# Performance work log

Measured on AMD Instinct MI355X. Metric: run time of the kernel, lower is better.

The kernel has to match this reference:

```python
import jax, jax.numpy as jnp
import numpy as np
import math

B, C, L, D = 64, 21, 8192, 512
KG, KP = 25, 15  # gaussian decomp kernel, phase-corrector kernel (both odd)
PI = math.pi


def _reflect_pad(x, k):
    # x: [B, C, T]; torch 'same' reflect padding: left = k//2, right = k-1-k//2
    pl = k // 2
    return jnp.pad(x, ((0, 0), (0, 0), (pl, k - 1 - pl)), mode='reflect')


def _depthwise_conv1d(x, w):
    # x: [B, C, T_pad], w: [C, 1, k]  (cross-correlation, groups=C, VALID)
    return jax.lax.conv_general_dilated(
        x, w, window_strides=(1,), padding='VALID',
        dimension_numbers=('NCH', 'OIH', 'NCH'),
        feature_group_count=x.shape[1])


def _phase_unwrap(phase):
    # phase: [B, L, C]; unwrap along time axis=1 (matches torch implementation)
    d = jnp.diff(phase, axis=1)
    d_mod = jnp.mod(d + PI, 2.0 * PI) - PI
    d_mod = jnp.where((d_mod == -PI) & (d > 0), PI, d_mod)
    correction = jnp.cumsum(d_mod - d, axis=1)
    return jnp.concatenate([phase[:, :1, :], phase[:, 1:, :] + correction], axis=1)


def _analytic_signal(x):
    # scipy.signal.hilbert along axis=1; x: [B, L, C], L even
    n = x.shape[1]
    h = np.zeros(n, dtype=np.float32)
    h[0] = 1.0
    h[n // 2] = 1.0
    h[1:n // 2] = 2.0
    Xf = jnp.fft.fft(x, axis=1)
    return jnp.fft.ifft(Xf * jnp.asarray(h)[None, :, None], axis=1)


def setup_inputs() -> dict:
    key = jax.random.key(0)
    ks = jax.random.split(key, 4)
    return {
        'x_input': jax.random.normal(ks[0], (B, C, L), jnp.float32),
        'x_w': jax.random.normal(ks[1], (L, D), jnp.float32) / np.sqrt(L).astype(np.float32),
        'x_b': jnp.zeros((D,), jnp.float32),
        'i_w': jax.random.normal(ks[2], (L, D), jnp.float32) / np.sqrt(L).astype(np.float32),
        'i_b': jnp.zeros((D,), jnp.float32),
        'log_sigma': jnp.full((C,), math.log(3.0), jnp.float32),
        'pc_weight': jax.random.normal(ks[3], (C, 1, KP), jnp.float32) * 0.01,
        'pc_strength': jnp.asarray(0.2, jnp.float32),
        'alpha_log': jnp.zeros((C,), jnp.float32),
        'phi0': jnp.zeros((C,), jnp.float32),
        'beta1_log': jnp.asarray(0.0, jnp.float32),
        'beta2_log': jnp.asarray(0.0, jnp.float32),
    }


def reference(x_input, x_w, x_b, i_w, i_b, log_sigma, pc_weight, pc_strength,
              alpha_log, phi0, beta1_log, beta2_log):
    # x_input: [B, C, L]
    x_out = jax.nn.gelu(x_input @ x_w + x_b, approximate=False)  # [B, C, D]

    # --- decomp_Gaussian (depthwise gaussian low-pass) ---
    half = KG // 2
    idx = jnp.arange(-half, half + 1, dtype=x_input.dtype)
    sigma = jnp.exp(log_sigma)[:, None, None] + 1e-6            # [C,1,1]
    g = jnp.exp(-(idx[None, None, :] ** 2) / (2.0 * sigma * sigma))
    g = g / (g.sum(axis=-1, keepdims=True) + 1e-12)             # [C,1,KG]
    trend_ch = _depthwise_conv1d(_reflect_pad(x_input, KG), g)  # [B,C,L]
    seasonal = (x_input - trend_ch).transpose(0, 2, 1)          # [B,L,C]
    trend = trend_ch.transpose(0, 2, 1)                         # [B,L,C]

    # --- TSCoupler ---
    # hilbert_transform uses .detach() in the original -> stop_gradient
    z = _analytic_signal(jax.lax.stop_gradient(seasonal))
    phase = jnp.arctan2(z.imag, z.real)                         # [B,L,C]
    phase_u = _phase_unwrap(phase)

    # ZeroMeanPhaseCorrector
    w = pc_weight - pc_weight.mean(axis=-1, keepdims=True)
    delta = _depthwise_conv1d(_reflect_pad(phase_u.transpose(0, 2, 1), KP), w)
    phi_corr = phase_u + jnp.tanh(pc_strength) * delta.transpose(0, 2, 1)
    phi_corr = phi_corr + phi0[None, None, :]

    T_clamped = jnp.clip(trend, -10.0, 10.0)
    beta1 = jax.nn.softplus(beta1_log) + 1e-6
    beta2 = jax.nn.softplus(beta2_log) + 1e-6
    A_raw = beta1 * jnp.log1p(jnp.exp(beta2 * T_clamped))       # [B,L,C]
    alpha = jax.nn.softplus(alpha_log)[None, None, :] + 1e-6    # [1,1,C]
    A_t = alpha * A_raw[0]                                      # [1,L,C]  (batch-0 indexing, as in source)
    I = (A_t * jnp.cos(phi_corr)).transpose(0, 2, 1)            # [B,C,L]

    I_coupled = jax.nn.gelu(I @ i_w + i_b, approximate=False)   # [B,C,D]
    return (x_out, I_coupled)
```

## Files before the change

kernel.cpp:

```cpp
#include <hip/hip_runtime.h>
#include <hip/hip_bf16.h>
#include <math.h>

#define LMAX 8192
#define KGAUSS 25

#define PI_F 3.14159265358979323846f
#define TWO_PI_F 6.28318530717958647692f

typedef __hip_bfloat16 bf16;
typedef unsigned short u16;
typedef short bf16x8 __attribute__((ext_vector_type(8)));
typedef float f32x4 __attribute__((ext_vector_type(4)));

__device__ __forceinline__ float b2f(bf16 v) { return __bfloat162float(v); }
__device__ __forceinline__ bf16 f2b(float v) { return __float2bfloat16(v); }
__device__ __forceinline__ float rdv(const void* p, long i, int isb) {
  return isb ? b2f(((const bf16*)p)[i]) : ((const float*)p)[i];
}

__device__ __forceinline__ void async16(const void* g, void* l) {
#if __has_builtin(__builtin_amdgcn_global_load_lds)
  __builtin_amdgcn_global_load_lds((const __attribute__((address_space(1))) void*)g,
                                   (__attribute__((address_space(3))) void*)l, 16, 0, 0);
#else
  *(uint4*)l = *(const uint4*)g;
#endif
}

__device__ __forceinline__ float2 f2add(float2 a, float2 b) {
  return make_float2(a.x + b.x, a.y + b.y);
}
__device__ __forceinline__ float2 f2sub(float2 a, float2 b) {
  return make_float2(a.x - b.x, a.y - b.y);
}
__device__ __forceinline__ float2 cmulc(float2 x, float2 w) {
  return make_float2(x.x * w.x + x.y * w.y, x.y * w.x - x.x * w.y);
}
__device__ __forceinline__ float2 cmul(float2 x, float2 w) {
  return make_float2(x.x * w.x - x.y * w.y, x.x * w.y + x.y * w.x);
}
#define ZI(i) ((i) ^ (((i) >> 4) & 15))
#define XS(i) ((i) ^ (((i) >> 5) & 31))

__global__ void k_params(const void* xb, const void* ib, const void* ls, const void* pw,
                         const void* al, const void* ph, const void* ps, const void* b1,
                         const void* b2, float* pf, int* flag, float2* tw,
                         int D, int C, int KP, int L) {
  unsigned wls = ((const unsigned*)ls)[0];
  int isb = ((wls >> 16) == (wls & 0xffffu)) ? 1 : 0;
  int blk = blockIdx.x, t = threadIdx.x;
  if (blk < 64) {
    int i = blk * 256 + t;
    if (i == 0) flag[0] = isb;
    float v = 0.0f;
    if (i < D)                              v = rdv(xb, i, isb);
    else if (i >= 2048 && i < 2048 + D)     v = rdv(ib, i - 2048, isb);
    else if (i >= 4096 && i < 4096 + C)     v = rdv(ls, i - 4096, isb);
    else if (i >= 4352 && i < 4352 + C*KP)  v = rdv(pw, i - 4352, isb);
    else if (i >= 8448 && i < 8448 + C)     v = rdv(al, i - 8448, isb);
    else if (i >= 8704 && i < 8704 + C)     v = rdv(ph, i - 8704, isb);
    else if (i == 8960)                     v = rdv(ps, 0, isb);
    else if (i == 8961)                     v = rdv(b1, 0, isb);
    else if (i == 8962)                     v = rdv(b2, 0, isb);
    pf[i] = v;
  } else {
    int j = (blk - 64) * 256 + t;
    if (j < L / 2) {
      double a = 6.283185307179586476925286766559 * (double)j / (double)L;
      tw[j] = make_float2((float)cos(a), (float)sin(a));
    }
  }
}

__global__ __launch_bounds__(256) void k_transpose(const void* __restrict__ in,
    bf16* __restrict__ out, const int* __restrict__ flag, int K, int N) {
  __shared__ u16 tile[64][65];
  int isb = *flag;
  int r0 = blockIdx.x * 64, c0 = blockIdx.y * 64;
  int t = threadIdx.x;
#pragma unroll
  for (int i = 0; i < 16; ++i) {
    int idx = t + i * 256;
    int r = idx >> 6, cc = idx & 63;
    int gr = r0 + r; gr = gr < K ? gr : K - 1;
    int gc = c0 + cc; gc = gc < N ? gc : N - 1;
    size_t gi = (size_t)gr * N + gc;
    u16 v;
    if (isb) v = ((const u16*)in)[gi];
    else { bf16 h = f2b(((const float*)in)[gi]); v = *(u16*)&h; }
    tile[r][cc] = v;
  }
  __syncthreads();
#pragma unroll
  for (int i = 0; i < 16; ++i) {
    int idx = t + i * 256;
    int a = idx >> 6, bb = idx & 63;
    if (c0 + a < N && r0 + bb < K)
      ((u16*)out)[(size_t)(c0 + a) * K + (r0 + bb)] = tile[bb][a];
  }
}

__global__ __launch_bounds__(256, 4) void k_decomp32(const void* __restrict__ x,
    const int* __restrict__ flag, const float* __restrict__ pf,
    float* __restrict__ seasonal, float* __restrict__ trend0,
    bf16* __restrict__ Xb, int C, int L) {
  __shared__ float xs[LMAX + LMAX / 32];
  int bc = blockIdx.x, c = bc % C, b = bc / C;
  int t = threadIdx.x;
  int isb = *flag;
  for (int i = t; i < L; i += 256) {
    float xv = rdv(x, (size_t)bc * L + i, isb);
    xs[i + (i >> 5)] = xv;
    Xb[(size_t)bc * L + i] = f2b(xv);
  }
  float sigma = expf(pf[4096 + c]) + 1e-6f;
  float inv2s2 = 1.0f / (2.0f * sigma * sigma);
  float g[KGAUSS];
  float gs = 0.0f;
#pragma unroll
  for (int j = 0; j < KGAUSS; ++j) {
    float d = (float)(j - 12);
    float vv = expf(-(d * d) * inv2s2);
    g[j] = vv; gs += vv;
  }
  float ginv = 1.0f / (gs + 1e-12f);
#pragma unroll
  for (int j = 0; j < KGAUSS; ++j) g[j] *= ginv;
  __syncthreads();
  const int base = 32 * t;
  float v[56];
#pragma unroll
  for (int m = 0; m < 56; ++m) {
    int idx = base + m - 12;
    idx = idx < 0 ? -idx : (idx >= L ? 2 * L - 2 - idx : idx);
    v[m] = xs[idx + (idx >> 5)];
  }
  __syncthreads();
  const int sb = 33 * t;
  float aA = 0.0f, ab1 = 0.0f, ab2 = 0.0f;
  if (b == 0) {
    aA  = log1pf(expf(pf[8448 + c])) + 1e-6f;
    ab1 = log1pf(expf(pf[8961])) + 1e-6f;
    ab2 = log1pf(expf(pf[8962])) + 1e-6f;
  }
  float* trow = trend0 + (size_t)c * L;
#pragma unroll
  for (int ii = 0; ii < 32; ++ii) {
    float acc = 0.0f;
#pragma unroll
    for (int j = 0; j < KGAUSS; ++j) acc = fmaf(g[j], v[ii + j], acc);
    xs[sb + ii] = v[ii + 12] - acc;
    if (b == 0) {
      float T = fminf(10.0f, fmaxf(-10.0f, acc));
      trow[base + ii] = aA * (ab1 * log1pf(expf(ab2 * T)));
    }
  }
  __syncthreads();
  for (int i = t; i < L; i += 256)
    seasonal[(size_t)bc * L + i] = xs[i + (i >> 5)];
}

__global__ __launch_bounds__(256) void k_decomp(const void* __restrict__ x,
    const int* __restrict__ flag, const float* __restrict__ pf,
    float* __restrict__ seasonal, float* __restrict__ trend0,
    bf16* __restrict__ Xb, int C, int L) {
  __shared__ float xs[LMAX];
  int bc = blockIdx.x;
  int c = bc % C, b = bc / C;
  int t = threadIdx.x;
  int isb = *flag;
  for (int i = t; i < L; i += 256) {
    float xv = rdv(x, (size_t)bc * L + i, isb);
    xs[i] = xv;
    Xb[(size_t)bc * L + i] = f2b(xv);
  }
  float sigma = expf(pf[4096 + c]) + 1e-6f;
  float inv2s2 = 1.0f / (2.0f * sigma * sigma);
  float g[KGAUSS];
  float gs = 0.0f;
  for (int j = 0; j < KGAUSS; ++j) {
    float d = (float)(j - 12);
    float v = expf(-(d * d) * inv2s2);
    g[j] = v; gs += v;
  }
  float ginv = 1.0f / (gs + 1e-12f);
  for (int j = 0; j < KGAUSS; ++j) g[j] *= ginv;
  float aA  = log1pf(expf(pf[8448 + c])) + 1e-6f;
  float ab1 = log1pf(expf(pf[8961])) + 1e-6f;
  float ab2 = log1pf(expf(pf[8962])) + 1e-6f;
  __syncthreads();
  for (int i = t; i < L; i += 256) {
    float acc = 0.0f;
#pragma unroll
    for (int j = 0; j < KGAUSS; ++j) {
      int idx = i + j - 12;
      idx = idx < 0 ? -idx : (idx >= L ? 2 * L - 2 - idx : idx);
      acc += g[j] * xs[idx];
    }
    seasonal[(size_t)bc * L + i] = xs[i] - acc;
    if (b == 0) {
      float T = fminf(10.0f, fmaxf(-10.0f, acc));
      trend0[(size_t)c * L + i] = aA * (ab1 * log1pf(expf(ab2 * T)));
    }
  }
}

__global__ __launch_bounds__(512, 4) void k_hilbert_unwrap(
    const float* __restrict__ sp, const float2* __restrict__ tw,
    const float* __restrict__ amp, const float* __restrict__ pf,
    bf16* __restrict__ I, int C, int L, int lg, long M) {
  __shared__ float2 z[LMAX];
  float* P = (float*)z;
  long r0 = 2L * blockIdx.x;
  int has1 = (r0 + 1 < M) ? 1 : 0;
  const float* row0 = sp + (size_t)r0 * L;
  const float* row1 = row0 + (has1 ? (size_t)L : 0);
  const int t = threadIdx.x;
  const int T = 512;
  const int nq = L >> 3;

  for (int s = lg; s >= 4; s -= 3) {
    const int h4 = 1 << (s - 3);
    for (int q = t; q < nq; q += T) {
      int pos = q & (h4 - 1);
      int base = ((q >> (s - 3)) << s) + pos;
      float2 E0, E1, E2, E3, E4, E5, E6, E7;
      if (s == lg) {
        int i;
        i = base;          E0 = make_float2(row0[i], has1 ? row1[i] : 0.0f);
        i = base + h4;     E1 = make_float2(row0[i], has1 ? row1[i] : 0.0f);
        i = base + 2*h4;   E2 = make_float2(row0[i], has1 ? row1[i] : 0.0f);
        i = base + 3*h4;   E3 = make_float2(row0[i], has1 ? row1[i] : 0.0f);
        i = base + 4*h4;   E4 = make_float2(row0[i], has1 ? row1[i] : 0.0f);
        i = base + 5*h4;   E5 = make_float2(row0[i], has1 ? row1[i] : 0.0f);
        i = base + 6*h4;   E6 = make_float2(row0[i], has1 ? row1[i] : 0.0f);
        i = base + 7*h4;   E7 = make_float2(row0[i], has1 ? row1[i] : 0.0f);
      } else {
        E0 = z[ZI(base)];          E1 = z[ZI(base + h4)];
        E2 = z[ZI(base + 2*h4)];   E3 = z[ZI(base + 3*h4)];
        E4 = z[ZI(base + 4*h4)];   E5 = z[ZI(base + 5*h4)];
        E6 = z[ZI(base + 6*h4)];   E7 = z[ZI(base + 7*h4)];
      }
      float2 wa0 = tw[pos << (lg - s)];
      float2 wa1 = tw[(pos + h4) << (lg - s)];
      float2 wa2 = tw[(pos + 2*h4) << (lg - s)];
      float2 wa3 = tw[(pos + 3*h4) << (lg - s)];
      float2 wb0 = tw[pos << (lg - s + 1)];
      float2 wb1 = tw[(pos + h4) << (lg - s + 1)];
      float2 wc0 = tw[pos << (lg - s + 2)];
      float2 A0 = f2add(E0, E4), B0 = cmulc(f2sub(E0, E4), wa0);
      float2 A1 = f2add(E1, E5), B1 = cmulc(f2sub(E1, E5), wa1);
      float2 A2 = f2add(E2, E6), B2 = cmulc(f2sub(E2, E6), wa2);
      float2 A3 = f2add(E3, E7), B3 = cmulc(f2sub(E3, E7), wa3);
      float2 C0 = f2add(A0, A2), C2 = cmulc(f2sub(A0, A2), wb0);
      float2 C1 = f2add(A1, A3), C3 = cmulc(f2sub(A1, A3), wb1);
      float2 D0 = f2add(B0, B2), D2 = cmulc(f2sub(B0, B2), wb0);
      float2 D1 = f2add(B1, B3), D3 = cmulc(f2sub(B1, B3), wb1);
      z[ZI(base)]          = f2add(C0, C1);
      z[ZI(base + h4)]     = cmulc(f2sub(C0, C1), wc0);
      z[ZI(base + 2*h4)]   = f2add(C2, C3);
      z[ZI(base + 3*h4)]   = cmulc(f2sub(C2, C3), wc0);
      z[ZI(base + 4*h4)]   = f2add(D0, D1);
      z[ZI(base + 5*h4)]   = cmulc(f2sub(D0, D1), wc0);
      z[ZI(base + 6*h4)]   = f2add(D2, D3);
      z[ZI(base + 7*h4)]   = cmulc(f2sub(D2, D3), wc0);
    }
    __syncthreads();
  }
  {
    const float s1 = 1.0f / (float)L, s2 = 2.0f / (float)L;
    const int h = L >> 1;
    for (int q = t; q < (L >> 1); q += T) {
      int i0 = 2 * q, i1 = i0 + 1;
      float2 a = z[ZI(i0)], b = z[ZI(i1)];
      float2 u0 = f2add(a, b), u1 = f2sub(a, b);
      int k0 = (int)(__brev((unsigned)i0) >> (32 - lg));
      int k1 = (int)(__brev((unsigned)i1) >> (32 - lg));
      float sc0 = (k0 == 0 || k0 == h) ? s1 : (k0 < h ? s2 : 0.0f);
      float sc1 = (k1 == 0 || k1 == h) ? s1 : (k1 < h ? s2 : 0.0f);
      u0.x *= sc0; u0.y *= sc0; u1.x *= sc1; u1.y *= sc1;
      z[ZI(i0)] = f2add(u0, u1);
      z[ZI(i1)] = f2sub(u0, u1);
    }
  }
  __syncthreads();
  for (int s = 2; s + 2 <= lg - 3; s += 3) {
    const int h = 1 << (s - 1);
    for (int q = t; q < nq; q += T) {
      int pos = q & (h - 1);
      int base = ((q >> (s - 1)) << (s + 2)) + pos;
      float2 E0 = z[ZI(base)],         E1 = z[ZI(base + h)];
      float2 E2 = z[ZI(base + 2*h)],   E3 = z[ZI(base + 3*h)];
      float2 E4 = z[ZI(base + 4*h)],   E5 = z[ZI(base + 5*h)];
      float2 E6 = z[ZI(base + 6*h)],   E7 = z[ZI(base + 7*h)];
      float2 w0  = tw[pos << (lg - s)];
      float2 w10 = tw[pos << (lg - s - 1)];
      float2 w11 = tw[(pos + h) << (lg - s - 1)];
      float2 w20 = tw[pos << (lg - s - 2)];
      float2 w21 = tw[(pos + h) << (lg - s - 2)];
      float2 w22 = tw[(pos + 2*h) << (lg - s - 2)];
      float2 w23 = tw[(pos + 3*h) << (lg - s - 2)];
      float2 c;
      c = cmul(E1, w0); float2 A0 = f2add(E0, c), A1 = f2sub(E0, c);
      c = cmul(E3, w0); float2 A2 = f2add(E2, c), A3 = f2sub(E2, c);
      c = cmul(E5, w0); float2 A4 = f2add(E4, c), A5 = f2sub(E4, c);
      c = cmul(E7, w0); float2 A6 = f2add(E6, c), A7 = f2sub(E6, c);
      c = cmul(A2, w10); float2 B0 = f2add(A0, c), B2 = f2sub(A0, c);
      c = cmul(A3, w11); float2 B1 = f2add(A1, c), B3 = f2sub(A1, c);
      c = cmul(A6, w10); float2 B4 = f2add(A4, c), B6 = f2sub(A4, c);
      c = cmul(A7, w11); float2 B5 = f2add(A5, c), B7 = f2sub(A5, c);
      float2 F0, F1, F2, F3, F4, F5, F6, F7;
      c = cmul(B4, w20); F0 = f2add(B0, c); F4 = f2sub(B0, c);
      c = cmul(B5, w21); F1 = f2add(B1, c); F5 = f2sub(B1, c);
      c = cmul(B6, w22); F2 = f2add(B2, c); F6 = f2sub(B2, c);
      c = cmul(B7, w23); F3 = f2add(B3, c); F7 = f2sub(B3, c);
      z[ZI(base)]        = F0; z[ZI(base + h)]    = F1;
      z[ZI(base + 2*h)]  = F2; z[ZI(base + 3*h)]  = F3;
      z[ZI(base + 4*h)]  = F4; z[ZI(base + 5*h)]  = F5;
      z[ZI(base + 6*h)]  = F6; z[ZI(base + 7*h)]  = F7;
    }
    __syncthreads();
  }
  {
    const int s = lg - 2;
    const int h = 1 << (s - 1);
    float2 Ea[2][8];
    int bs[2];
#pragma unroll
    for (int it = 0; it < 2; ++it) {
      int q = t + it * T;
      int pos = q & (h - 1);
      int base = ((q >> (s - 1)) << (s + 2)) + pos;
      bs[it] = base;
      Ea[it][0] = z[ZI(base)];         Ea[it][1] = z[ZI(base + h)];
      Ea[it][2] = z[ZI(base + 2*h)];   Ea[it][3] = z[ZI(base + 3*h)];
      Ea[it][4] = z[ZI(base + 4*h)];   Ea[it][5] = z[ZI(base + 5*h)];
      Ea[it][6] = z[ZI(base + 6*h)];   Ea[it][7] = z[ZI(base + 7*h)];
    }
    __syncthreads();
#pragma unroll
    for (int it = 0; it < 2; ++it) {
      int q = t + it * T;
      int pos = q & (h - 1);
      int base = bs[it];
      float2 w0  = tw[pos << (lg - s)];
      float2 w10 = tw[pos << (lg - s - 1)];
      float2 w11 = tw[(pos + h) << (lg - s - 1)];
      float2 w20 = tw[pos << (lg - s - 2)];
      float2 w21 = tw[(pos + h) << (lg - s - 2)];
      float2 w22 = tw[(pos + 2*h) << (lg - s - 2)];
      float2 w23 = tw[(pos + 3*h) << (lg - s - 2)];
      float2 c;
      c = cmul(Ea[it][1], w0); float2 A0 = f2add(Ea[it][0], c), A1 = f2sub(Ea[it][0], c);
      c = cmul(Ea[it][3], w0); float2 A2 = f2add(Ea[it][2], c), A3 = f2sub(Ea[it][2], c);
      c = cmul(Ea[it][5], w0); float2 A4 = f2add(Ea[it][4], c), A5 = f2sub(Ea[it][4], c);
      c = cmul(Ea[it][7], w0); float2 A6 = f2add(Ea[it][6], c), A7 = f2sub(Ea[it][6], c);
      c = cmul(A2, w10); float2 B0 = f2add(A0, c), B2 = f2sub(A0, c);
      c = cmul(A3, w11); float2 B1 = f2add(A1, c), B3 = f2sub(A1, c);
      c = cmul(A6, w10); float2 B4 = f2add(A4, c), B6 = f2sub(A4, c);
      c = cmul(A7, w11); float2 B5 = f2add(A5, c), B7 = f2sub(A5, c);
      float2 F[8];
      c = cmul(B4, w20); F[0] = f2add(B0, c); F[4] = f2sub(B0, c);
      c = cmul(B5, w21); F[1] = f2add(B1, c); F[5] = f2sub(B1, c);
      c = cmul(B6, w22); F[2] = f2add(B2, c); F[6] = f2sub(B2, c);
      c = cmul(B7, w23); F[3] = f2add(B3, c); F[7] = f2sub(B3, c);
#pragma unroll
      for (int j = 0; j < 8; ++j) {
        int i = base + j * h;
        float xa = row0[i];
        float xb = has1 ? row1[i] : 0.0f;
        float ha = F[j].y - xb;
        float hb = xa - F[j].x;
        P[XS(i)] = atan2f(ha, xa);
        P[L + XS(i)] = has1 ? atan2f(hb, xb) : 0.0f;
      }
    }
  }
  __syncthreads();
  {
    int tr = t & 255, row = t >> 8;
    int rowoff = row ? L : 0;
    int c = (int)((r0 + row) % C);
    int sb32 = 32 * tr;
    float v[32];
#pragma unroll
    for (int ii = 0; ii < 32; ++ii) v[ii] = P[rowoff + XS(sb32 + ii)];
    float prev0 = (tr > 0) ? P[rowoff + XS(sb32 - 1)] : 0.0f;
    __syncthreads();
    int run = 0;
    {
      float prev = prev0;
#pragma unroll
      for (int ii = 0; ii < 32; ++ii) {
        float cur = v[ii];
        if (ii > 0 || tr > 0) {
          float d = cur - prev;
          int k = (int)floorf((d + PI_F) * (1.0f / TWO_PI_F));
          float m = d - TWO_PI_F * (float)k;
          if (m == -PI_F && d > 0.0f) k -= 1;
          run -= k;
        }
        prev = cur;
        v[ii] = cur + TWO_PI_F * (float)run;
      }
    }
    int lane = t & 63, w = t >> 6;
    int inc = run;
#pragma unroll
    for (int off2 = 1; off2 < 64; off2 <<= 1) {
      int n = __shfl_up(inc, off2);
      if (lane >= off2) inc += n;
    }
    int* iP = (int*)P;
    if (lane == 63) iP[w] = inc;
    __syncthreads();
    int base = inc - run;
    int rowbase = row * 4;
    for (int ww = rowbase; ww < w; ++ww) base += iP[ww];
    __syncthreads();
    float fb = TWO_PI_F * (float)base;
#pragma unroll
    for (int ii = 0; ii < 32; ++ii) v[ii] += fb;
#pragma unroll
    for (int ii = 0; ii < 32; ++ii) P[rowoff + XS(sb32 + ii)] = v[ii];
    __syncthreads();
    float hl[7], hr[7];
#pragma unroll
    for (int m = 0; m < 7; ++m)
      hl[m] = (tr == 0) ? v[7 - m] : P[rowoff + XS(sb32 - 7 + m)];
#pragma unroll
    for (int m = 0; m < 7; ++m)
      hr[m] = (tr == 255) ? v[30 - m] : P[rowoff + XS(sb32 + 32 + m)];
    __syncthreads();
    float wz[15];
    float mean = 0.0f;
#pragma unroll
    for (int j = 0; j < 15; ++j) { wz[j] = pf[4352 + c * 15 + j]; mean += wz[j]; }
    mean *= (1.0f / 15.0f);
#pragma unroll
    for (int j = 0; j < 15; ++j) wz[j] -= mean;
    float tanh_s = tanhf(pf[8960]);
    float phi0c = pf[8704 + c];
#pragma unroll
    for (int ii = 0; ii < 32; ++ii) {
      float delta = 0.0f;
#pragma unroll
      for (int j = 0; j < 15; ++j) {
        int idx = ii + j - 7;
        float u = (idx < 0) ? hl[idx + 7] : (idx >= 32 ? hr[idx - 32] : v[idx]);
        delta = fmaf(wz[j], u, delta);
      }
      float phi = v[ii] + tanh_s * delta + phi0c;
      P[rowoff + XS(sb32 + ii)] = cosf(phi);
    }
    __syncthreads();
    const float* ar0 = amp + (size_t)(r0 % C) * L;
    const float* ar1 = amp + (size_t)((r0 + 1) % C) * L;
    bf16* I0 = I + (size_t)r0 * L;
    bf16* I1 = I0 + L;
    for (int i = t; i < L; i += 512) {
      I0[i] = f2b(ar0[i] * P[XS(i)]);
      if (has1) I1[i] = f2b(ar1[i] * P[L + XS(i)]);
    }
  }
}

__global__ __launch_bounds__(512, 4) void k_hilbert8(float* __restrict__ sp,
    const float2* __restrict__ tw, int L, int lg, long M) {
  __shared__ float2 z[LMAX];
  long r0 = 2L * blockIdx.x;
  int has1 = (r0 + 1 < M) ? 1 : 0;
  float* row0 = sp + (size_t)r0 * L;
  float* row1 = row0 + (has1 ? (size_t)L : 0);
  const int t = threadIdx.x;
  const int T = 512;
  const int nq = L >> 3;

  for (int s = lg; s >= 4; s -= 3) {
    const int h4 = 1 << (s - 3);
    for (int q = t; q < nq; q += T) {
      int pos = q & (h4 - 1);
      int base = ((q >> (s - 3)) << s) + pos;
      float2 E0, E1, E2, E3, E4, E5, E6, E7;
      if (s == lg) {
        int i;
        i = base;          E0 = make_float2(row0[i], has1 ? row1[i] : 0.0f);
        i = base + h4;     E1 = make_float2(row0[i], has1 ? row1[i] : 0.0f);
        i = base + 2*h4;   E2 = make_float2(row0[i], has1 ? row1[i] : 0.0f);
        i = base + 3*h4;   E3 = make_float2(row0[i], has1 ? row1[i] : 0.0f);
        i = base + 4*h4;   E4 = make_float2(row0[i], has1 ? row1[i] : 0.0f);
        i = base + 5*h4;   E5 = make_float2(row0[i], has1 ? row1[i] : 0.0f);
        i = base + 6*h4;   E6 = make_float2(row0[i], has1 ? row1[i] : 0.0f);
        i = base + 7*h4;   E7 = make_float2(row0[i], has1 ? row1[i] : 0.0f);
      } else {
        E0 = z[ZI(base)];          E1 = z[ZI(base + h4)];
        E2 = z[ZI(base + 2*h4)];   E3 = z[ZI(base + 3*h4)];
        E4 = z[ZI(base + 4*h4)];   E5 = z[ZI(base + 5*h4)];
        E6 = z[ZI(base + 6*h4)];   E7 = z[ZI(base + 7*h4)];
      }
      float2 wa0 = tw[pos << (lg - s)];
      float2 wa1 = tw[(pos + h4) << (lg - s)];
      float2 wa2 = tw[(pos + 2*h4) << (lg - s)];
      float2 wa3 = tw[(pos + 3*h4) << (lg - s)];
      float2 wb0 = tw[pos << (lg - s + 1)];
      float2 wb1 = tw[(pos + h4) << (lg - s + 1)];
      float2 wc0 = tw[pos << (lg - s + 2)];
      float2 A0 = f2add(E0, E4), B0 = cmulc(f2sub(E0, E4), wa0);
      float2 A1 = f2add(E1, E5), B1 = cmulc(f2sub(E1, E5), wa1);
      float2 A2 = f2add(E2, E6), B2 = cmulc(f2sub(E2, E6), wa2);
      float2 A3 = f2add(E3, E7), B3 = cmulc(f2sub(E3, E7), wa3);
      float2 C0 = f2add(A0, A2), C2 = cmulc(f2sub(A0, A2), wb0);
      float2 C1 = f2add(A1, A3), C3 = cmulc(f2sub(A1, A3), wb1);
      float2 D0 = f2add(B0, B2), D2 = cmulc(f2sub(B0, B2), wb0);
      float2 D1 = f2add(B1, B3), D3 = cmulc(f2sub(B1, B3), wb1);
      z[ZI(base)]          = f2add(C0, C1);
      z[ZI(base + h4)]     = cmulc(f2sub(C0, C1), wc0);
      z[ZI(base + 2*h4)]   = f2add(C2, C3);
      z[ZI(base + 3*h4)]   = cmulc(f2sub(C2, C3), wc0);
      z[ZI(base + 4*h4)]   = f2add(D0, D1);
      z[ZI(base + 5*h4)]   = cmulc(f2sub(D0, D1), wc0);
      z[ZI(base + 6*h4)]   = f2add(D2, D3);
      z[ZI(base + 7*h4)]   = cmulc(f2sub(D2, D3), wc0);
    }
    __syncthreads();
  }
  {
    const float s1 = 1.0f / (float)L, s2 = 2.0f / (float)L;
    const int h = L >> 1;
    for (int q = t; q < (L >> 1); q += T) {
      int i0 = 2 * q, i1 = i0 + 1;
      float2 a = z[ZI(i0)], b = z[ZI(i1)];
      float2 u0 = f2add(a, b), u1 = f2sub(a, b);
      int k0 = (int)(__brev((unsigned)i0) >> (32 - lg));
      int k1 = (int)(__brev((unsigned)i1) >> (32 - lg));
      float sc0 = (k0 == 0 || k0 == h) ? s1 : (k0 < h ? s2 : 0.0f);
      float sc1 = (k1 == 0 || k1 == h) ? s1 : (k1 < h ? s2 : 0.0f);
      u0.x *= sc0; u0.y *= sc0; u1.x *= sc1; u1.y *= sc1;
      z[ZI(i0)] = f2add(u0, u1);
      z[ZI(i1)] = f2sub(u0, u1);
    }
  }
  __syncthreads();
  for (int s = 2; s + 2 <= lg; s += 3) {
    const int h = 1 << (s - 1);
    const int last = (s + 2 == lg) ? 1 : 0;
    for (int q = t; q < nq; q += T) {
      int pos = q & (h - 1);
      int base = ((q >> (s - 1)) << (s + 2)) + pos;
      float2 E0 = z[ZI(base)],         E1 = z[ZI(base + h)];
      float2 E2 = z[ZI(base + 2*h)],   E3 = z[ZI(base + 3*h)];
      float2 E4 = z[ZI(base + 4*h)],   E5 = z[ZI(base + 5*h)];
      float2 E6 = z[ZI(base + 6*h)],   E7 = z[ZI(base + 7*h)];
      float2 w0  = tw[pos << (lg - s)];
      float2 w10 = tw[pos << (lg - s - 1)];
      float2 w11 = tw[(pos + h) << (lg - s - 1)];
      float2 w20 = tw[pos << (lg - s - 2)];
      float2 w21 = tw[(pos + h) << (lg - s - 2)];
      float2 w22 = tw[(pos + 2*h) << (lg - s - 2)];
      float2 w23 = tw[(pos + 3*h) << (lg - s - 2)];
      float2 c;
      c = cmul(E1, w0); float2 A0 = f2add(E0, c), A1 = f2sub(E0, c);
      c = cmul(E3, w0); float2 A2 = f2add(E2, c), A3 = f2sub(E2, c);
      c = cmul(E5, w0); float2 A4 = f2add(E4, c), A5 = f2sub(E4, c);
      c = cmul(E7, w0); float2 A6 = f2add(E6, c), A7 = f2sub(E6, c);
      c = cmul(A2, w10); float2 B0 = f2add(A0, c), B2 = f2sub(A0, c);
      c = cmul(A3, w11); float2 B1 = f2add(A1, c), B3 = f2sub(A1, c);
      c = cmul(A6, w10); float2 B4 = f2add(A4, c), B6 = f2sub(A4, c);
      c = cmul(A7, w11); float2 B5 = f2add(A5, c), B7 = f2sub(A5, c);
      float2 F0, F1, F2, F3, F4, F5, F6, F7;
      c = cmul(B4, w20); F0 = f2add(B0, c); F4 = f2sub(B0, c);
      c = cmul(B5, w21); F1 = f2add(B1, c); F5 = f2sub(B1, c);
      c = cmul(B6, w22); F2 = f2add(B2, c); F6 = f2sub(B2, c);
      c = cmul(B7, w23); F3 = f2add(B3, c); F7 = f2sub(B3, c);
      if (last) {
        float2 ov[8] = {F0, F1, F2, F3, F4, F5, F6, F7};
#pragma unroll
        for (int j = 0; j < 8; ++j) {
          int i = base + j * h;
          float xa = row0[i];
          float xb = has1 ? row1[i] : 0.0f;
          float ha = ov[j].y - xb;
          float hb = xa - ov[j].x;
          row0[i] = atan2f(ha, xa);
          if (has1) row1[i] = atan2f(hb, xb);
        }
      } else {
        z[ZI(base)]        = F0; z[ZI(base + h)]    = F1;
        z[ZI(base + 2*h)]  = F2; z[ZI(base + 3*h)]  = F3;
        z[ZI(base + 4*h)]  = F4; z[ZI(base + 5*h)]  = F5;
        z[ZI(base + 6*h)]  = F6; z[ZI(base + 7*h)]  = F7;
      }
    }
    if (!last) __syncthreads();
  }
}

__global__ __launch_bounds__(512, 4) void k_hilbert4(float* __restrict__ sp,
    const float2* __restrict__ tw, int L, int lg, long M) {
  __shared__ float2 z[LMAX];
  long r0 = 2L * blockIdx.x;
  int has1 = (r0 + 1 < M) ? 1 : 0;
  float* row0 = sp + (size_t)r0 * L;
  float* row1 = row0 + (has1 ? (size_t)L : 0);
  const int t = threadIdx.x;
  const int T = 512;
  const int nq = L >> 2;

  {
    const int s = lg;
    const int h = 1 << (s - 1), h2 = h >> 1;
    for (int q = t; q < nq; q += T) {
      int pos = q & (h2 - 1);
      int base = ((q >> (s - 2)) << s) + pos;
      int i0 = base, i1 = base + h2, i2 = base + h, i3 = base + h + h2;
      float2 e0 = make_float2(row0[i0], has1 ? row1[i0] : 0.0f);
      float2 e1 = make_float2(row0[i1], has1 ? row1[i1] : 0.0f);
      float2 e2 = make_float2(row0[i2], has1 ? row1[i2] : 0.0f);
      float2 e3 = make_float2(row0[i3], has1 ? row1[i3] : 0.0f);
      float2 wa = tw[pos << (lg - s)];
      float2 wb = tw[(pos + h2) << (lg - s)];
      float2 wc = tw[pos << (lg - s + 1)];
      float2 t0 = f2add(e0, e2), t2 = cmulc(f2sub(e0, e2), wa);
      float2 t1 = f2add(e1, e3), t3 = cmulc(f2sub(e1, e3), wb);
      z[ZI(i0)] = f2add(t0, t1);
      z[ZI(i1)] = cmulc(f2sub(t0, t1), wc);
      z[ZI(i2)] = f2add(t2, t3);
      z[ZI(i3)] = cmulc(f2sub(t2, t3), wc);
    }
  }
  __syncthreads();
  for (int s = lg - 2; s >= 2; s -= 2) {
    const int h = 1 << (s - 1), h2 = h >> 1;
    for (int q = t; q < nq; q += T) {
      int pos = q & (h2 - 1);
      int base = ((q >> (s - 2)) << s) + pos;
      int i0 = base, i1 = base + h2, i2 = base + h, i3 = base + h + h2;
      float2 e0 = z[ZI(i0)], e1 = z[ZI(i1)], e2 = z[ZI(i2)], e3 = z[ZI(i3)];
      float2 wa = tw[pos << (lg - s)];
      float2 wb = tw[(pos + h2) << (lg - s)];
      float2 wc = tw[pos << (lg - s + 1)];
      float2 t0 = f2add(e0, e2), t2 = cmulc(f2sub(e0, e2), wa);
      float2 t1 = f2add(e1, e3), t3 = cmulc(f2sub(e1, e3), wb);
      z[ZI(i0)] = f2add(t0, t1);
      z[ZI(i1)] = cmulc(f2sub(t0, t1), wc);
      z[ZI(i2)] = f2add(t2, t3);
      z[ZI(i3)] = cmulc(f2sub(t2, t3), wc);
    }
    __syncthreads();
  }
  {
    const float s1 = 1.0f / (float)L, s2 = 2.0f / (float)L;
    const int h = L >> 1;
    if (lg & 1) {
      for (int q = t; q < (L >> 1); q += T) {
        int i0 = 2 * q, i1 = i0 + 1;
        float2 a = z[ZI(i0)], b = z[ZI(i1)];
        float2 u0 = f2add(a, b), u1 = f2sub(a, b);
        int k0 = (int)(__brev((unsigned)i0) >> (32 - lg));
        int k1 = (int)(__brev((unsigned)i1) >> (32 - lg));
        float sc0 = (k0 == 0 || k0 == h) ? s1 : (k0 < h ? s2 : 0.0f);
        float sc1 = (k1 == 0 || k1 == h) ? s1 : (k1 < h ? s2 : 0.0f);
        u0.x *= sc0; u0.y *= sc0; u1.x *= sc1; u1.y *= sc1;
        z[ZI(i0)] = f2add(u0, u1);
        z[ZI(i1)] = f2sub(u0, u1);
      }
    } else {
      for (int p = t; p < L; p += T) {
        int k = (int)(__brev((unsigned)p) >> (32 - lg));
        float sc = (k == 0 || k == h) ? s1 : (k < h ? s2 : 0.0f);
        float2 v = z[ZI(p)];
        v.x *= sc; v.y *= sc;
        z[ZI(p)] = v;
      }
    }
  }
  __syncthreads();
  const int s0 = (lg & 1) ? 2 : 1;
  for (int s = s0; s + 1 <= lg - 2; s += 2) {
    const int hs = 1 << (s - 1);
    for (int q = t; q < nq; q += T) {
      int pos = q & (hs - 1);
      int base = ((q >> (s - 1)) << (s + 1)) + pos;
      int i0 = base, i1 = base + hs, i2 = base + 2 * hs, i3 = base + 3 * hs;
      float2 e0 = z[ZI(i0)], e1 = z[ZI(i1)], e2 = z[ZI(i2)], e3 = z[ZI(i3)];
      float2 wa = tw[pos << (lg - s)];
      float2 wb = tw[pos << (lg - s - 1)];
      float2 wcc = tw[(pos + hs) << (lg - s - 1)];
      float2 c1 = cmul(e1, wa);
      float2 t0 = f2add(e0, c1), t1 = f2sub(e0, c1);
      float2 d1 = cmul(e3, wa);
      float2 t2 = f2add(e2, d1), t3 = f2sub(e2, d1);
      c1 = cmul(t2, wb);
      float2 o0 = f2add(t0, c1), o2 = f2sub(t0, c1);
      d1 = cmul(t3, wcc);
      float2 o1 = f2add(t1, d1), o3 = f2sub(t1, d1);
      z[ZI(i0)] = o0; z[ZI(i1)] = o1; z[ZI(i2)] = o2; z[ZI(i3)] = o3;
    }
    __syncthreads();
  }
  {
    const int s = lg - 1;
    const int hs = 1 << (s - 1);
    for (int q = t; q < nq; q += T) {
      int pos = q & (hs - 1);
      int base = ((q >> (s - 1)) << (s + 1)) + pos;
      int i0 = base, i1 = base + hs, i2 = base + 2 * hs, i3 = base + 3 * hs;
      float2 e0 = z[ZI(i0)], e1 = z[ZI(i1)], e2 = z[ZI(i2)], e3 = z[ZI(i3)];
      float2 wa = tw[pos << (lg - s)];
      float2 wb = tw[pos << (lg - s - 1)];
      float2 wcc = tw[(pos + hs) << (lg - s - 1)];
      float2 c1 = cmul(e1, wa);
      float2 t0 = f2add(e0, c1), t1 = f2sub(e0, c1);
      float2 d1 = cmul(e3, wa);
      float2 t2 = f2add(e2, d1), t3 = f2sub(e2, d1);
      c1 = cmul(t2, wb);
      float2 o0 = f2add(t0, c1), o2 = f2sub(t0, c1);
      d1 = cmul(t3, wcc);
      float2 o1 = f2add(t1, d1), o3 = f2sub(t1, d1);
      int idx[4] = {i0, i1, i2, i3};
      float2 ov[4] = {o0, o1, o2, o3};
#pragma unroll
      for (int j = 0; j < 4; ++j) {
        int i = idx[j];
        float xa = row0[i];
        float xb = has1 ? row1[i] : 0.0f;
        float2 w = ov[j];
        float ha = w.y - xb;
        float hb = xa - w.x;
        row0[i] = atan2f(ha, xa);
        if (has1) row1[i] = atan2f(hb, xb);
      }
    }
  }
}

__global__ __launch_bounds__(256, 4) void k_unwrap_I32(
    const float* __restrict__ phase_all, const float* __restrict__ amp,
    const float* __restrict__ pf, bf16* __restrict__ I, int C, int L) {
  __shared__ float p[LMAX + LMAX / 32];
  __shared__ int wsum[8];
  int bc = blockIdx.x, c = bc % C;
  int t = threadIdx.x;
  const float* prow = phase_all + (size_t)bc * L;
  for (int i = t; i < L; i += 256) p[i + (i >> 5)] = prow[i];
  __syncthreads();
  const int sbase = 33 * t;
  float v[32];
#pragma unroll
  for (int ii = 0; ii < 32; ++ii) v[ii] = p[sbase + ii];
  float prev = (t > 0) ? p[sbase - 2] : 0.0f;
  int run = 0;
#pragma unroll
  for (int ii = 0; ii < 32; ++ii) {
    float cur = v[ii];
    if (ii > 0 || t > 0) {
      float d = cur - prev;
      int k = (int)floorf((d + PI_F) * (1.0f / TWO_PI_F));
      float m = d - TWO_PI_F * (float)k;
      if (m == -PI_F && d > 0.0f) k -= 1;
      run -= k;
    }
    prev = cur;
    v[ii] = cur + TWO_PI_F * (float)run;
  }
  int lane = t & 63, w = t >> 6;
  int inc = run;
#pragma unroll
  for (int off = 1; off < 64; off <<= 1) {
    int n = __shfl_up(inc, off);
    if (lane >= off) inc += n;
  }
  if (lane == 63) wsum[w] = inc;
  __syncthreads();
  int base = inc - run;
  for (int ww = 0; ww < w; ++ww) base += wsum[ww];
  float fb = TWO_PI_F * (float)base;
#pragma unroll
  for (int ii = 0; ii < 32; ++ii) v[ii] += fb;
#pragma unroll
  for (int ii = 0; ii < 32; ++ii) p[sbase + ii] = v[ii];
  __syncthreads();
  float hl[7], hr[7];
#pragma unroll
  for (int m = 0; m < 7; ++m)
    hl[m] = (t == 0) ? v[7 - m] : p[sbase - 8 + m];
#pragma unroll
  for (int m = 0; m < 7; ++m)
    hr[m] = (t == 255) ? v[30 - m] : p[sbase + 33 + m];
  __syncthreads();
  float wz[15];
  float mean = 0.0f;
#pragma unroll
  for (int j = 0; j < 15; ++j) { wz[j] = pf[4352 + c * 15 + j]; mean += wz[j]; }
  mean /= 15.0f;
#pragma unroll
  for (int j = 0; j < 15; ++j) wz[j] -= mean;
  float tanh_s = tanhf(pf[8960]);
  float phi0c = pf[8704 + c];
#pragma unroll
  for (int ii = 0; ii < 32; ++ii) {
    float delta = 0.0f;
#pragma unroll
    for (int j = 0; j < 15; ++j) {
      int idx = ii + j - 7;
      float u = (idx < 0) ? hl[idx + 7] : (idx >= 32 ? hr[idx - 32] : v[idx]);
      delta = fmaf(wz[j], u, delta);
    }
    float phi = v[ii] + tanh_s * delta + phi0c;
    p[sbase + ii] = cosf(phi);
  }
  __syncthreads();
  const float* arow = amp + (size_t)c * L;
  bf16* Irow = I + (size_t)bc * L;
  for (int i = t; i < L; i += 256)
    Irow[i] = f2b(arow[i] * p[i + (i >> 5)]);
}

__global__ __launch_bounds__(256) void k_unwrap_I(const float* __restrict__ phase_all,
    const float* __restrict__ amp, const float* __restrict__ pf,
    bf16* __restrict__ I, int C, int L, int KP) {
  __shared__ float p[LMAX];
  __shared__ int ksum[256];
  int bc = blockIdx.x;
  int c = bc % C;
  int t = threadIdx.x;
  int chunk = L >> 8;
  const float* prow = phase_all + (size_t)bc * L;
  for (int i = t; i < L; i += 256) p[i] = prow[i];
  __syncthreads();
  int start = t * chunk;
  float prev0 = (t > 0) ? p[start - 1] : 0.0f;
  int kacc = 0;
  {
    float prev = prev0;
    for (int ii = 0; ii < chunk; ++ii) {
      int i = start + ii;
      float cur = p[i];
      if (i > 0) {
        float d = cur - prev;
        int k = (int)floorf((d + PI_F) * (1.0f / TWO_PI_F));
        float m = d - TWO_PI_F * (float)k;
        if (m == -PI_F && d > 0.0f) k -= 1;
        kacc -= k;
      }
      prev = cur;
    }
  }
  ksum[t] = kacc;
  __syncthreads();
  if (t == 0) {
    int run = 0;
    for (int i = 0; i < 256; ++i) { int v = ksum[i]; ksum[i] = run; run += v; }
  }
  __syncthreads();
  {
    int run = ksum[t];
    float prev = prev0;
    for (int ii = 0; ii < chunk; ++ii) {
      int i = start + ii;
      float cur = p[i];
      if (i > 0) {
        float d = cur - prev;
        int k = (int)floorf((d + PI_F) * (1.0f / TWO_PI_F));
        float m = d - TWO_PI_F * (float)k;
        if (m == -PI_F && d > 0.0f) k -= 1;
        run -= k;
      }
      prev = cur;
      p[i] = cur + TWO_PI_F * (float)run;
    }
  }
  __syncthreads();
  float wz[32];
  float mean = 0.0f;
  for (int j = 0; j < KP; ++j) { wz[j] = pf[4352 + c * KP + j]; mean += wz[j]; }
  mean /= (float)KP;
  for (int j = 0; j < KP; ++j) wz[j] -= mean;
  int hk = KP / 2;
  float tanh_s = tanhf(pf[8960]);
  float phi0c = pf[8704 + c];
  const float* arow = amp + (size_t)c * L;
  bf16* Irow = I + (size_t)bc * L;
  for (int i = t; i < L; i += 256) {
    float delta = 0.0f;
    for (int j = 0; j < KP; ++j) {
      int idx = i + j - hk;
      idx = idx < 0 ? -idx : (idx >= L ? 2 * L - 2 - idx : idx);
      delta = fmaf(wz[j], p[idx], delta);
    }
    float phi = p[i] + tanh_s * delta + phi0c;
    Irow[i] = f2b(arow[i] * cosf(phi));
  }
}

__global__ __launch_bounds__(256) void k_gemm_sk(const bf16* __restrict__ A0,
    const bf16* __restrict__ A1, const bf16* __restrict__ B0,
    const bf16* __restrict__ B1, float* __restrict__ part,
    int M, int L, int D, int KS, int KC) {
  __shared__ __align__(16) u16 As[128 * 32];
  __shared__ __align__(16) u16 Bs[128 * 32];
  int zz = blockIdx.z;
  int g = zz / KS, ks = zz - g * KS;
  const u16* Ag = (const u16*)(g ? A1 : A0);
  const u16* Bg = (const u16*)(g ? B1 : B0);
  int m0 = blockIdx.x * 128, n0 = blockIdx.y * 128;
  int t = threadIdx.x;
  int l = t & 63, w = t >> 6;
  int wm = (w >> 1) * 64, wn = (w & 1) * 64;
  int lr = l & 15, lq = l >> 4;
  f32x4 acc[4][4];
  f32x4 z4 = 0.0f;
  for (int i = 0; i < 4; ++i)
    for (int j = 0; j < 4; ++j) acc[i][j] = z4;

  int kbeg = ks * KC, kend = kbeg + KC;
  for (int k0 = kbeg; k0 < kend; k0 += 32) {
#pragma unroll
    for (int q = 0; q < 2; ++q) {
      int chunk = q * 256 + t;
      int row = chunk >> 2, kc = chunk & 3;
      int ar = m0 + row; ar = ar < M ? ar : M - 1;
      int br = n0 + row; br = br < D ? br : D - 1;
      async16(Ag + (size_t)ar * L + (k0 + kc * 8), As + chunk * 8);
      async16(Bg + (size_t)br * L + (k0 + kc * 8), Bs + chunk * 8);
    }
    __syncthreads();
    bf16x8 af[4], bfr[4];
#pragma unroll
    for (int i = 0; i < 4; ++i) {
      af[i]  = *(const bf16x8*)(As + (wm + i * 16 + lr) * 32 + lq * 8);
      bfr[i] = *(const bf16x8*)(Bs + (wn + i * 16 + lr) * 32 + lq * 8);
    }
#pragma unroll
    for (int i = 0; i < 4; ++i)
#pragma unroll
      for (int j = 0; j < 4; ++j)
        acc[i][j] = __builtin_amdgcn_mfma_f32_16x16x32_bf16(af[i], bfr[j], acc[i][j], 0, 0, 0);
    __syncthreads();
  }
  float* pbase = part + (size_t)zz * M * D;
#pragma unroll
  for (int i = 0; i < 4; ++i) {
    int rowb = m0 + wm + i * 16 + lq * 4;
#pragma unroll
    for (int j = 0; j < 4; ++j) {
      int gcol = n0 + wn + j * 16 + lr;
      if (gcol < D) {
#pragma unroll
        for (int r = 0; r < 4; ++r) {
          int grow = rowb + r;
          if (grow < M)
            pbase[(size_t)grow * D + gcol] = acc[i][j][r];
        }
      }
    }
  }
}

__global__ __launch_bounds__(256) void k_reduce(const float* __restrict__ part,
    const float* __restrict__ pf, float* __restrict__ out, long MD, int D, int KS) {
  long idx = (long)blockIdx.x * 256 + threadIdx.x;
  if (idx >= 2 * MD) return;
  int g = (int)(idx / MD);
  long r = idx - (long)g * MD;
  const float* p = part + (size_t)g * KS * MD + r;
  float s = 0.0f;
  for (int ks = 0; ks < KS; ++ks) s += p[(size_t)ks * MD];
  int d = (int)(r % (long)D);
  float v = s + pf[g * 2048 + d];
  out[idx] = 0.5f * v * (1.0f + erff(v * 0.70710678118654752f));
}

static inline int cdiv_i(long a, long b) { return (int)((a + b - 1) / b); }

extern "C" void kernel_launch(void* const* d_in, const int* in_sizes, int n_in,
                              void* d_out, int out_size, void* d_ws, size_t ws_size,
                              hipStream_t stream) {
  long B = 64, C = 21, L = 8192, D = 512, KP = 15;
  if (n_in == 12) {
    long Sx = in_sizes[0], Sw = in_sizes[1], Sb = in_sizes[2];
    long Sls = in_sizes[5], Spw = in_sizes[6];
    if (Sb > 0 && Sw % Sb == 0 && Sls > 0 && Spw % Sls == 0) {
      long Lc = Sw / Sb, KPc = Spw / Sls;
      if (Lc >= 256 && Lc <= LMAX && !(Lc & (Lc - 1)) && (KPc & 1) && KPc <= 31 &&
          Sx % (Sls * Lc) == 0) {
        L = Lc; D = Sb; C = Sls; KP = KPc; B = Sx / (Sls * Lc);
      }
    }
  }
  long M = B * C;
  int lg = 0; while ((1L << lg) < L) ++lg;

  const void* x_input = d_in[0];
  const void* x_w     = d_in[1];
  const void* x_b     = d_in[2];
  const void* i_w     = d_in[3];
  const void* i_b     = d_in[4];
  const void* lsg     = d_in[5];
  const void* pw      = d_in[6];
  const void* ps      = d_in[7];
  const void* al      = d_in[8];
  const void* ph      = d_in[9];
  const void* b1      = d_in[10];
  const void* b2      = d_in[11];

  char* ws = (char*)d_ws;
  size_t off = 0;
  auto take = [&](size_t bytes) { size_t o = off; off = (off + bytes + 255) & ~(size_t)255; return o; };
  float*  seasonal = (float*)(ws + take((size_t)M * L * 4));
  float*  trend0   = (float*)(ws + take((size_t)C * L * 4));
  bf16*   Ibuf     = (bf16*)(ws + take((size_t)M * L * 2));
  float2* tw       = (float2*)(ws + take((size_t)(L / 2) * 8));
  float*  pf       = (float*)(ws + take(65536));
  int*    flag     = (int*)(ws + take(256));
  bf16*   Xb       = (bf16*)(ws + take((size_t)M * L * 2));
  bf16*   Btx      = (bf16*)(ws + take((size_t)D * L * 2));
  bf16*   Bti      = (bf16*)(ws + take((size_t)D * L * 2));
  if (ws_size < off) return;

  int KS = 8;
  while (KS > 1 && ((L % ((long)KS * 32)) != 0 || 2L * KS * D > L)) KS >>= 1;
  float* out0 = (float*)d_out;
  float* part = (2L * KS * D <= L) ? seasonal : out0;
  int KC = (int)(L / KS);

  k_params<<<64 + cdiv_i(L / 2, 256), 256, 0, stream>>>(
      x_b, i_b, lsg, pw, al, ph, ps, b1, b2, pf, flag, tw,
      (int)D, (int)C, (int)KP, (int)L);

  k_transpose<<<dim3(cdiv_i(L, 64), cdiv_i(D, 64)), 256, 0, stream>>>(x_w, Btx, flag,
                                                                      (int)L, (int)D);
  k_transpose<<<dim3(cdiv_i(L, 64), cdiv_i(D, 64)), 256, 0, stream>>>(i_w, Bti, flag,
                                                                      (int)L, (int)D);

  if (L == 8192)
    k_decomp32<<<(int)M, 256, 0, stream>>>(x_input, flag, pf, seasonal, trend0, Xb,
                                           (int)C, (int)L);
  else
    k_decomp<<<(int)M, 256, 0, stream>>>(x_input, flag, pf, seasonal, trend0, Xb,
                                         (int)C, (int)L);

  bool fused = (L == 8192 && KP == 15 && ((lg - 1) % 3 == 0));
  if (fused) {
    k_hilbert_unwrap<<<cdiv_i(M, 2), 512, 0, stream>>>(
        seasonal, tw, trend0, pf, Ibuf, (int)C, (int)L, lg, M);
  } else {
    if ((lg - 1) % 3 == 0)
      k_hilbert8<<<cdiv_i(M, 2), 512, 0, stream>>>(seasonal, tw, (int)L, lg, M);
    else
      k_hilbert4<<<cdiv_i(M, 2), 512, 0, stream>>>(seasonal, tw, (int)L, lg, M);
    if (L == 8192 && KP == 15)
      k_unwrap_I32<<<(int)M, 256, 0, stream>>>(seasonal, trend0, pf, Ibuf, (int)C, (int)L);
    else
      k_unwrap_I<<<(int)M, 256, 0, stream>>>(seasonal, trend0, pf, Ibuf, (int)C, (int)L,
                                             (int)KP);
  }

  k_gemm_sk<<<dim3(cdiv_i(M, 128), cdiv_i(D, 128), 2 * KS), 256, 0, stream>>>(
      Xb, Ibuf, Btx, Bti, part, (int)M, (int)L, (int)D, KS, KC);
  k_reduce<<<cdiv_i(2 * M * D, 256), 256, 0, stream>>>(part, pf, out0, M * D, (int)D, KS);
}
```

Baseline: 374.2 us.

## Double-buffer GEMM LDS tiles, merge weight transposes, vectorize split-K reduce

The split-K GEMM now double-buffers its A/B LDS tiles. The next k-slice's async global-to-LDS loads are issued before computing on the current buffer, and one barrier per iteration is removed. The two weight transpose launches are merged into one launch using blockIdx.z, and the split-K reduction with GELU is vectorized to float4 loads and stores. These target memory latency in the GEMM, launch overhead, and reduce bandwidth efficiency, at the cost of doubled LDS usage per block.

```diff
diff --git a/kernel.cpp b/kernel.cpp
--- a/kernel.cpp
+++ b/kernel.cpp
@@ -73,10 +73,13 @@
   }
 }
 
-__global__ __launch_bounds__(256) void k_transpose(const void* __restrict__ in,
-    bf16* __restrict__ out, const int* __restrict__ flag, int K, int N) {
+__global__ __launch_bounds__(256) void k_transpose2(const void* __restrict__ in0,
+    const void* __restrict__ in1, bf16* __restrict__ out0, bf16* __restrict__ out1,
+    const int* __restrict__ flag, int K, int N) {
   __shared__ u16 tile[64][65];
   int isb = *flag;
+  const void* in = blockIdx.z ? in1 : in0;
+  bf16* out = blockIdx.z ? out1 : out0;
   int r0 = blockIdx.x * 64, c0 = blockIdx.y * 64;
   int t = threadIdx.x;
 #pragma unroll
@@ -898,8 +901,8 @@
     const bf16* __restrict__ A1, const bf16* __restrict__ B0,
     const bf16* __restrict__ B1, float* __restrict__ part,
     int M, int L, int D, int KS, int KC) {
-  __shared__ __align__(16) u16 As[128 * 32];
-  __shared__ __align__(16) u16 Bs[128 * 32];
+  __shared__ __align__(16) u16 As[2][128 * 32];
+  __shared__ __align__(16) u16 Bs[2][128 * 32];
   int zz = blockIdx.z;
   int g = zz / KS, ks = zz - g * KS;
   const u16* Ag = (const u16*)(g ? A1 : A0);
@@ -914,30 +917,37 @@
   for (int i = 0; i < 4; ++i)
     for (int j = 0; j < 4; ++j) acc[i][j] = z4;
 
+  int row = t >> 2, kc = t & 3;
+  int ar = m0 + row; ar = ar < M ? ar : M - 1;
+  int br = n0 + row; br = br < D ? br : D - 1;
+  int row2 = (256 + t) >> 2, kc2 = t & 3;
+  int ar2 = m0 + row2; ar2 = ar2 < M ? ar2 : M - 1;
+  int br2 = n0 + row2; br2 = br2 < D ? br2 : D - 1;
+
   int kbeg = ks * KC, kend = kbeg + KC;
+  auto STAGE = [&](int buf, int k0) {
+    async16(Ag + (size_t)ar * L + (k0 + kc * 8), &As[buf][t * 8]);
+    async16(Bg + (size_t)br * L + (k0 + kc * 8), &Bs[buf][t * 8]);
+    async16(Ag + (size_t)ar2 * L + (k0 + kc2 * 8), &As[buf][(256 + t) * 8]);
+    async16(Bg + (size_t)br2 * L + (k0 + kc2 * 8), &Bs[buf][(256 + t) * 8]);
+  };
+  STAGE(0, kbeg);
+  int cur = 0;
   for (int k0 = kbeg; k0 < kend; k0 += 32) {
-#pragma unroll
-    for (int q = 0; q < 2; ++q) {
-      int chunk = q * 256 + t;
-      int row = chunk >> 2, kc = chunk & 3;
-      int ar = m0 + row; ar = ar < M ? ar : M - 1;
-      int br = n0 + row; br = br < D ? br : D - 1;
-      async16(Ag + (size_t)ar * L + (k0 + kc * 8), As + chunk * 8);
-      async16(Bg + (size_t)br * L + (k0 + kc * 8), Bs + chunk * 8);
-    }
-    __syncthreads();
+    __syncthreads();
+    if (k0 + 32 < kend) STAGE(cur ^ 1, k0 + 32);
     bf16x8 af[4], bfr[4];
 #pragma unroll
     for (int i = 0; i < 4; ++i) {
-      af[i]  = *(const bf16x8*)(As + (wm + i * 16 + lr) * 32 + lq * 8);
-      bfr[i] = *(const bf16x8*)(Bs + (wn + i * 16 + lr) * 32 + lq * 8);
+      af[i]  = *(const bf16x8*)(&As[cur][(wm + i * 16 + lr) * 32 + lq * 8]);
+      bfr[i] = *(const bf16x8*)(&Bs[cur][(wn + i * 16 + lr) * 32 + lq * 8]);
     }
 #pragma unroll
     for (int i = 0; i < 4; ++i)
 #pragma unroll
       for (int j = 0; j < 4; ++j)
         acc[i][j] = __builtin_amdgcn_mfma_f32_16x16x32_bf16(af[i], bfr[j], acc[i][j], 0, 0, 0);
-    __syncthreads();
+    cur ^= 1;
   }
   float* pbase = part + (size_t)zz * M * D;
 #pragma unroll
@@ -956,6 +966,31 @@
       }
     }
   }
+}
+
+__global__ __launch_bounds__(256) void k_reduce4(const float* __restrict__ part,
+    const float* __restrict__ pf, float* __restrict__ out, long MD, int D, int KS) {
+  long i4 = ((long)blockIdx.x * 256 + threadIdx.x) * 4;
+  if (i4 >= 2 * MD) return;
+  int g = (int)(i4 / MD);
+  long r = i4 - (long)g * MD;
+  const float* p = part + (size_t)g * KS * MD + r;
+  float4 s = make_float4(0.f, 0.f, 0.f, 0.f);
+  for (int ks = 0; ks < KS; ++ks) {
+    float4 v = *(const float4*)(p + (size_t)ks * MD);
+    s.x += v.x; s.y += v.y; s.z += v.z; s.w += v.w;
+  }
+  int d = (int)(r % (long)D);
+  const float* bias = pf + g * 2048 + d;
+  float vv[4] = {s.x, s.y, s.z, s.w};
+  float4 o;
+  float* po = (float*)&o;
+#pragma unroll
+  for (int j = 0; j < 4; ++j) {
+    float v = vv[j] + bias[j];
+    po[j] = 0.5f * v * (1.0f + erff(v * 0.70710678118654752f));
+  }
+  *(float4*)(out + i4) = o;
 }
 
 __global__ __launch_bounds__(256) void k_reduce(const float* __restrict__ part,
@@ -1029,10 +1064,8 @@
       x_b, i_b, lsg, pw, al, ph, ps, b1, b2, pf, flag, tw,
       (int)D, (int)C, (int)KP, (int)L);
 
-  k_transpose<<<dim3(cdiv_i(L, 64), cdiv_i(D, 64)), 256, 0, stream>>>(x_w, Btx, flag,
-                                                                      (int)L, (int)D);
-  k_transpose<<<dim3(cdiv_i(L, 64), cdiv_i(D, 64)), 256, 0, stream>>>(i_w, Bti, flag,
-                                                                      (int)L, (int)D);
+  k_transpose2<<<dim3(cdiv_i(L, 64), cdiv_i(D, 64), 2), 256, 0, stream>>>(
+      x_w, i_w, Btx, Bti, flag, (int)L, (int)D);
 
   if (L == 8192)
     k_decomp32<<<(int)M, 256, 0, stream>>>(x_input, flag, pf, seasonal, trend0, Xb,
@@ -1059,5 +1092,10 @@
 
   k_gemm_sk<<<dim3(cdiv_i(M, 128), cdiv_i(D, 128), 2 * KS), 256, 0, stream>>>(
       Xb, Ibuf, Btx, Bti, part, (int)M, (int)L, (int)D, KS, KC);
-  k_reduce<<<cdiv_i(2 * M * D, 256), 256, 0, stream>>>(part, pf, out0, M * D, (int)D, KS);
-}
+  if ((D % 4 == 0) && ((M * D) % 4 == 0))
+    k_reduce4<<<cdiv_i(2 * M * D / 4, 256), 256, 0, stream>>>(part, pf, out0, M * D,
+                                                              (int)D, KS);
+  else
+    k_reduce<<<cdiv_i(2 * M * D, 256), 256, 0, stream>>>(part, pf, out0, M * D,
+                                                         (int)D, KS);
+}
```

After: 357.2 us. 4.6% less time.
